# Kernel tuning notes

Hardware: AMD Instinct MI355X
Metric: run time of the kernel (lower is better)

Reference implementation:

```python
import jax, jax.numpy as jnp
import numpy as np

B, T, C, HS = 8, 4096, 128, 64
NEG_INF = -1e30  # stand-in for float('-inf') that is fp16/bf16-safe


def _rope(x, cos, sin):
    # x: [B, T, HS]; cos/sin: [T, HS//2]
    xr = x.reshape(*x.shape[:-1], HS // 2, 2)
    x0, x1 = xr[..., 0], xr[..., 1]
    # complex multiply (x0 + i x1) * (cos + i sin)
    o0 = x0 * cos - x1 * sin
    o1 = x0 * sin + x1 * cos
    return jnp.stack([o0, o1], axis=-1).reshape(x.shape)


def setup_inputs() -> dict:
    key = jax.random.key(0)
    k0, k1, k2, k3, k4 = jax.random.split(key, 5)
    x_text_emb = jax.random.normal(k0, (B, T, C), dtype=jnp.float32)
    Wq = jax.random.normal(k1, (C, HS), dtype=jnp.float32) * 0.02
    Wk = jax.random.normal(k2, (C, HS), dtype=jnp.float32) * 0.02
    Wv = jax.random.normal(k3, (C, HS), dtype=jnp.float32) * 0.02
    # RoPE frequencies: theta_i = 10000^{-2i/HS}, angles = pos * theta
    theta = 10000.0 ** (-jnp.arange(0, HS, 2, dtype=jnp.float32) / HS)  # [HS//2]
    angles = jnp.arange(T, dtype=jnp.float32)[:, None] * theta[None, :]  # [T, HS//2]
    freqs_cos = jnp.cos(angles)
    freqs_sin = jnp.sin(angles)
    # padding mask: ones for a valid prefix (length >= T//2 so no row is fully masked)
    lengths = jax.random.randint(k4, (B,), T // 2, T + 1)
    x_latex_mask = (jnp.arange(T)[None, :] < lengths[:, None]).astype(jnp.int32)
    return {"x_text_emb": x_text_emb, "Wq": Wq, "Wk": Wk, "Wv": Wv,
            "freqs_cos": freqs_cos, "freqs_sin": freqs_sin,
            "x_latex_mask": x_latex_mask}


def reference(x_text_emb, Wq, Wk, Wv, freqs_cos, freqs_sin, x_latex_mask):
    q = _rope(x_text_emb @ Wq, freqs_cos, freqs_sin)           # [B,T,HS]
    k = _rope(x_text_emb @ Wk, freqs_cos, freqs_sin)           # [B,T,HS]
    v = x_text_emb @ Wv                                        # [B,T,HS]
    # NOTE: source divides by sqrt(C) (embedding dim), not sqrt(head_size)
    wei = jnp.einsum('bqd,bkd->bqk', q, k) / jnp.sqrt(jnp.float32(C))  # [B,T,T]
    causal = jnp.tril(jnp.ones((T, T), dtype=bool))
    wei = jnp.where(causal[None, :, :], wei, NEG_INF)
    wei = jnp.where(x_latex_mask[:, None, :] != 0, wei, NEG_INF)
    softwei = jax.nn.softmax(wei, axis=-1)
    return jnp.einsum('bqk,bkd->bqd', softwei, v)              # [B,T,HS]
```

## Files before the change

kernel.cpp:

```cpp
#include <hip/hip_runtime.h>

#define B_ 8
#define T_ 4096
#define C_ 128
#define HS_ 64
#define NT16 (T_ / 16)

typedef _Float16 f16;
typedef _Float16 f16x8 __attribute__((ext_vector_type(8)));
typedef _Float16 f16x4 __attribute__((ext_vector_type(4)));
typedef float f32x4 __attribute__((ext_vector_type(4)));

#define MFMA32(a, b, c) __builtin_amdgcn_mfma_f32_16x16x32_f16(a, b, c, 0, 0, 0)
#define MFMA16(a, b, c) __builtin_amdgcn_mfma_f32_16x16x16f16(a, b, c, 0, 0, 0)


__global__ void k_prep(const float* __restrict__ Wq, const float* __restrict__ Wk,
                       const float* __restrict__ Wv, const int* __restrict__ msk,
                       f16* __restrict__ WT, f16* __restrict__ bias) {
    int idx = blockIdx.x * 256 + threadIdx.x;
    if (idx < 192 * C_) {
        int j = idx >> 7, c = idx & 127;
        const float* W = (j < 64) ? Wq : (j < 128 ? Wk : Wv);
        float v = W[c * HS_ + (j & 63)];
        if (j < 64) v *= 0.08838834764831845f;
        WT[idx] = (f16)v;
    } else {
        int e = idx - 192 * C_;
        if (e < B_ * T_) bias[e] = msk[e] ? (f16)0.0f : (f16)(-30000.0f);
    }
}

__global__ __launch_bounds__(256, 2) void k_qkv(const float* __restrict__ x,
        const f16* __restrict__ WT, const float* __restrict__ fcos,
        const float* __restrict__ fsin, f16* __restrict__ Qf,
        f16* __restrict__ Kf, f16* __restrict__ Vf) {
    const int b = blockIdx.y;
    const int tile64 = blockIdx.x >> 1, jh = blockIdx.x & 1;
    const int w = threadIdx.x >> 6, lane = threadIdx.x & 63;
    const int col = lane & 15, g = lane >> 4;
    const int t = tile64 * 64 + w * 16 + col;
    const int t16 = tile64 * 4 + w;
    const size_t fbase = ((size_t)(b * NT16) + t16) * 1024;

    f16x8 bx[4];
    const float* xrow = x + ((size_t)(b * T_ + t)) * C_;
#pragma unroll
    for (int cc = 0; cc < 4; ++cc) {
        float4 x0 = *(const float4*)(xrow + cc * 32 + g * 8);
        float4 x1 = *(const float4*)(xrow + cc * 32 + g * 8 + 4);
        f16x8 v;
        v[0] = (f16)x0.x; v[1] = (f16)x0.y; v[2] = (f16)x0.z; v[3] = (f16)x0.w;
        v[4] = (f16)x1.x; v[5] = (f16)x1.y; v[6] = (f16)x1.z; v[7] = (f16)x1.w;
        bx[cc] = v;
    }

#pragma unroll
    for (int jj = 0; jj < 6; ++jj) {
        const int jt = jh * 6 + jj;
        f32x4 acc = {0.f, 0.f, 0.f, 0.f};
#pragma unroll
        for (int cc = 0; cc < 4; ++cc) {
            f16x8 aw = *(const f16x8*)(WT + (size_t)(jt * 16 + col) * C_ + cc * 32 + g * 8);
            acc = MFMA32(aw, bx[cc], acc);
        }
        if (jt < 8) {
            const int j3 = jt & 3;
            const int hbase = j3 * 16 + g * 4;
            const int i0 = hbase >> 1;
            float2 c2 = *(const float2*)(fcos + t * 32 + i0);
            float2 s2 = *(const float2*)(fsin + t * 32 + i0);
            float o0 = acc[0] * c2.x - acc[1] * s2.x;
            float o1 = acc[0] * s2.x + acc[1] * c2.x;
            float o2 = acc[2] * c2.y - acc[3] * s2.y;
            float o3 = acc[2] * s2.y + acc[3] * c2.y;
            f16x4 st; st[0] = (f16)o0; st[1] = (f16)o1; st[2] = (f16)o2; st[3] = (f16)o3;
            const int h  = j3 >> 1;
            const int ga = ((j3 & 1) << 1) + (g >> 1);
            f16* dst = (jt < 4 ? Qf : Kf) + fbase + h * 512 + (ga * 16 + col) * 8 + (g & 1) * 4;
            *(f16x4*)dst = st;
        } else {
            const int mt = jt - 8;
            f16* vdst = Vf + fbase + mt * 256 + ((col >> 2) * 16 + g * 4) * 4 + (col & 3);
#pragma unroll
            for (int r = 0; r < 4; ++r) vdst[r * 4] = (f16)acc[r];
        }
    }
}

struct Tile32 {
    f16x8 k0[2], k1[2];
    f16x4 v[2][4];
    f16x4 bi[2];
};

__device__ __forceinline__ void load32(Tile32& t_, int it, const f16* __restrict__ kfb,
        const f16* __restrict__ vfb, const f16* __restrict__ brow, int lid, int g) {
#pragma unroll
    for (int s = 0; s < 2; ++s) {
        const f16* kt = kfb + (size_t)(it * 2 + s) * 1024;
        t_.k0[s] = *(const f16x8*)(kt + lid * 8);
        t_.k1[s] = *(const f16x8*)(kt + 512 + lid * 8);
        const f16* vt = vfb + (size_t)(it * 2 + s) * 1024;
#pragma unroll
        for (int mt = 0; mt < 4; ++mt)
            t_.v[s][mt] = *(const f16x4*)(vt + mt * 256 + lid * 4);
        t_.bi[s] = *(const f16x4*)(brow + it * 32 + s * 16 + g * 4);
    }
}

__device__ __forceinline__ void computeG(const Tile32& t_, int it, int qc, int g,
        f16x8 q0, f16x8 q1, float& m, float& lsum,
        f32x4& o0, f32x4& o1, f32x4& o2, f32x4& o3) {
    float sv[8];
#pragma unroll
    for (int s = 0; s < 2; ++s) {
        f32x4 sa = {0.f, 0.f, 0.f, 0.f};
        sa = MFMA32(t_.k0[s], q0, sa);
        sa = MFMA32(t_.k1[s], q1, sa);
        const int kbase = it * 32 + s * 16 + g * 4;
#pragma unroll
        for (int r = 0; r < 4; ++r) {
            float bb = (kbase + r <= qc) ? (float)t_.bi[s][r] : -1e30f;
            sv[s * 4 + r] = sa[r] + bb;
        }
    }
    float t0 = fmaxf(fmaxf(sv[0], sv[1]), fmaxf(sv[2], sv[3]));
    float t1 = fmaxf(fmaxf(sv[4], sv[5]), fmaxf(sv[6], sv[7]));
    float tm = fmaxf(t0, t1);
    tm = fmaxf(tm, __shfl_xor(tm, 16));
    tm = fmaxf(tm, __shfl_xor(tm, 32));
    const float mn = fmaxf(m, tm);
    const float sc = __expf(m - mn);
#pragma unroll
    for (int i = 0; i < 8; ++i) sv[i] = __expf(sv[i] - mn);
    float ts = ((sv[0] + sv[1]) + (sv[2] + sv[3])) + ((sv[4] + sv[5]) + (sv[6] + sv[7]));
    ts += __shfl_xor(ts, 16);
    ts += __shfl_xor(ts, 32);
    lsum = lsum * sc + ts;
    m = mn;
    o0 *= sc; o1 *= sc; o2 *= sc; o3 *= sc;
#pragma unroll
    for (int s = 0; s < 2; ++s) {
        f16x4 pf;
        pf[0] = (f16)sv[s * 4 + 0]; pf[1] = (f16)sv[s * 4 + 1];
        pf[2] = (f16)sv[s * 4 + 2]; pf[3] = (f16)sv[s * 4 + 3];
        o0 = MFMA16(t_.v[s][0], pf, o0);
        o1 = MFMA16(t_.v[s][1], pf, o1);
        o2 = MFMA16(t_.v[s][2], pf, o2);
        o3 = MFMA16(t_.v[s][3], pf, o3);
    }
}

__device__ __forceinline__ void writeG(float* __restrict__ out, int b, int qc, int g,
        float lsum, const f32x4& o0, const f32x4& o1, const f32x4& o2, const f32x4& o3) {
    const float inv = 1.0f / lsum;
    float* orow = out + ((size_t)(b * T_ + qc)) * HS_;
    float4 u;
    u.x = o0.x * inv; u.y = o0.y * inv; u.z = o0.z * inv; u.w = o0.w * inv;
    *(float4*)(orow + 0  + g * 4) = u;
    u.x = o1.x * inv; u.y = o1.y * inv; u.z = o1.z * inv; u.w = o1.w * inv;
    *(float4*)(orow + 16 + g * 4) = u;
    u.x = o2.x * inv; u.y = o2.y * inv; u.z = o2.z * inv; u.w = o2.w * inv;
    *(float4*)(orow + 32 + g * 4) = u;
    u.x = o3.x * inv; u.y = o3.y * inv; u.z = o3.z * inv; u.w = o3.w * inv;
    *(float4*)(orow + 48 + g * 4) = u;
}

__global__ __launch_bounds__(256, 1) void k_attn(const f16* __restrict__ Qf,
        const f16* __restrict__ Kf, const f16* __restrict__ Vf,
        const f16* __restrict__ bias, float* __restrict__ out) {
    const int b = blockIdx.y;
    const int xx = blockIdx.x;
    const int w = threadIdx.x >> 6, lane = threadIdx.x & 63;
    const int col = lane & 15, g = lane >> 4;
    const int lid = g * 16 + col;
    const int tqA = xx, tqB = 63 - xx;
    const int qcA = tqA * 64 + w * 16 + col;
    const int qcB = tqB * 64 + w * 16 + col;
    const int itA = (tqA * 64 + w * 16 + 15) >> 5;
    const int itB = (tqB * 64 + w * 16 + 15) >> 5;

    const f16* qfb = Qf + (size_t)(b * NT16) * 1024;
    const f16* kfb = Kf + (size_t)(b * NT16) * 1024;
    const f16* vfb = Vf + (size_t)(b * NT16) * 1024;
    const f16* brow = bias + (size_t)b * T_;

    const f16* qA = qfb + (size_t)(tqA * 4 + w) * 1024;
    f16x8 qA0 = *(const f16x8*)(qA + lid * 8);
    f16x8 qA1 = *(const f16x8*)(qA + 512 + lid * 8);
    const f16* qB = qfb + (size_t)(tqB * 4 + w) * 1024;
    f16x8 qB0 = *(const f16x8*)(qB + lid * 8);
    f16x8 qB1 = *(const f16x8*)(qB + 512 + lid * 8);

    float mA = -3.0e38f, lA = 0.f, mB = -3.0e38f, lB = 0.f;
    f32x4 oA0 = {0,0,0,0}, oA1 = {0,0,0,0}, oA2 = {0,0,0,0}, oA3 = {0,0,0,0};
    f32x4 oB0 = {0,0,0,0}, oB1 = {0,0,0,0}, oB2 = {0,0,0,0}, oB3 = {0,0,0,0};

    Tile32 A, Bt;
    load32(A, 0, kfb, vfb, brow, lid, g);
    int it = 0;
    for (; it + 2 <= itB; it += 2) {
        load32(Bt, it + 1, kfb, vfb, brow, lid, g);
        if (it <= itA) computeG(A, it, qcA, g, qA0, qA1, mA, lA, oA0, oA1, oA2, oA3);
        computeG(A, it, qcB, g, qB0, qB1, mB, lB, oB0, oB1, oB2, oB3);
        load32(A, it + 2, kfb, vfb, brow, lid, g);
        if (it + 1 <= itA) computeG(Bt, it + 1, qcA, g, qA0, qA1, mA, lA, oA0, oA1, oA2, oA3);
        computeG(Bt, it + 1, qcB, g, qB0, qB1, mB, lB, oB0, oB1, oB2, oB3);
    }
    if (it < itB) {
        load32(Bt, it + 1, kfb, vfb, brow, lid, g);
        if (it <= itA) computeG(A, it, qcA, g, qA0, qA1, mA, lA, oA0, oA1, oA2, oA3);
        computeG(A, it, qcB, g, qB0, qB1, mB, lB, oB0, oB1, oB2, oB3);
        if (it + 1 <= itA) computeG(Bt, it + 1, qcA, g, qA0, qA1, mA, lA, oA0, oA1, oA2, oA3);
        computeG(Bt, it + 1, qcB, g, qB0, qB1, mB, lB, oB0, oB1, oB2, oB3);
    } else {
        if (it <= itA) computeG(A, it, qcA, g, qA0, qA1, mA, lA, oA0, oA1, oA2, oA3);
        computeG(A, it, qcB, g, qB0, qB1, mB, lB, oB0, oB1, oB2, oB3);
    }

    writeG(out, b, qcA, g, lA, oA0, oA1, oA2, oA3);
    writeG(out, b, qcB, g, lB, oB0, oB1, oB2, oB3);
}

extern "C" void kernel_launch(void* const* d_in, const int* in_sizes, int n_in,
                              void* d_out, int out_size, void* d_ws, size_t ws_size,
                              hipStream_t stream) {
    const float* x    = (const float*)d_in[0];
    const float* Wq   = (const float*)d_in[1];
    const float* Wk   = (const float*)d_in[2];
    const float* Wv   = (const float*)d_in[3];
    const float* fcos = (const float*)d_in[4];
    const float* fsin = (const float*)d_in[5];
    const int*   msk  = (const int*)d_in[6];

    char* ws = (char*)d_ws;
    const size_t frag_bytes = (size_t)B_ * NT16 * 2048;
    f16* WT   = (f16*)ws;
    f16* bias = (f16*)(ws + (48 << 10));
    f16* Qf   = (f16*)(ws + (1 << 17));
    f16* Kf   = (f16*)(ws + (1 << 17) + frag_bytes);
    f16* Vf   = (f16*)(ws + (1 << 17) + 2 * frag_bytes);

    k_prep<<<224, 256, 0, stream>>>(Wq, Wk, Wv, msk, WT, bias);
    dim3 g1(T_ / 32, B_);
    k_qkv<<<g1, 256, 0, stream>>>(x, WT, fcos, fsin, Qf, Kf, Vf);
    dim3 g2(32, B_);
    k_attn<<<g2, 256, 0, stream>>>(Qf, Kf, Vf, bias, (float*)d_out);
}
```

Measured before the change: 171.7 us.

## Split KV range across waves in attention, stage QKV inputs in LDS

The attention kernel now launches 1024-thread blocks where each wave handles one query tile and half of its key range, merging the two partial softmax states through shared memory. This raises wave count and parallelism compared with two query tiles per wave processed serially. Along with this, the causal mask is applied only on the last key tile, and output rescaling is skipped when the running max does not change. The QKV projection now stages x and the weights in swizzled LDS, computes all 12 output tiles per block, and writes V through an LDS transpose for coalesced stores. The price is extra LDS use and a block-wide sync, and the attention loop no longer double-buffers its loads.

```diff
diff --git a/kernel.cpp b/kernel.cpp
--- a/kernel.cpp
+++ b/kernel.cpp
@@ -35,33 +35,57 @@
         const f16* __restrict__ WT, const float* __restrict__ fcos,
         const float* __restrict__ fsin, f16* __restrict__ Qf,
         f16* __restrict__ Kf, f16* __restrict__ Vf) {
+    __shared__ f16 xs[64 * 128];
+    __shared__ f16 wts[192 * 128];
+    __shared__ f16 vst[4][4][256];
+
     const int b = blockIdx.y;
-    const int tile64 = blockIdx.x >> 1, jh = blockIdx.x & 1;
-    const int w = threadIdx.x >> 6, lane = threadIdx.x & 63;
+    const int tid = threadIdx.x;
+    const int w = tid >> 6, lane = tid & 63;
     const int col = lane & 15, g = lane >> 4;
-    const int t = tile64 * 64 + w * 16 + col;
-    const int t16 = tile64 * 4 + w;
+
+    const float* xb = x + ((size_t)b * T_ + (size_t)blockIdx.x * 64) * C_;
+#pragma unroll
+    for (int k = 0; k < 8; ++k) {
+        int flat = tid * 4 + k * 1024;
+        float4 v4 = *(const float4*)(xb + flat);
+        f16x4 hv; hv[0] = (f16)v4.x; hv[1] = (f16)v4.y; hv[2] = (f16)v4.z; hv[3] = (f16)v4.w;
+        int row = flat >> 7, chB = (flat & 127) * 2;
+        int off = (row * 256 + chB) ^ ((row & 7) << 4);
+        *(f16x4*)((char*)xs + off) = hv;
+    }
+#pragma unroll
+    for (int k = 0; k < 12; ++k) {
+        int flat = tid * 8 + k * 2048;
+        f16x8 wv = *(const f16x8*)(WT + flat);
+        int row = flat >> 7, chB = (flat & 127) * 2;
+        int off = (row * 256 + chB) ^ ((row & 7) << 4);
+        *(f16x8*)((char*)wts + off) = wv;
+    }
+    __syncthreads();
+
+    const int t = blockIdx.x * 64 + w * 16 + col;
+    const int t16 = blockIdx.x * 4 + w;
     const size_t fbase = ((size_t)(b * NT16) + t16) * 1024;
 
     f16x8 bx[4];
-    const float* xrow = x + ((size_t)(b * T_ + t)) * C_;
-#pragma unroll
-    for (int cc = 0; cc < 4; ++cc) {
-        float4 x0 = *(const float4*)(xrow + cc * 32 + g * 8);
-        float4 x1 = *(const float4*)(xrow + cc * 32 + g * 8 + 4);
-        f16x8 v;
-        v[0] = (f16)x0.x; v[1] = (f16)x0.y; v[2] = (f16)x0.z; v[3] = (f16)x0.w;
-        v[4] = (f16)x1.x; v[5] = (f16)x1.y; v[6] = (f16)x1.z; v[7] = (f16)x1.w;
-        bx[cc] = v;
-    }
-
-#pragma unroll
-    for (int jj = 0; jj < 6; ++jj) {
-        const int jt = jh * 6 + jj;
+    {
+        const int row = w * 16 + col;
+#pragma unroll
+        for (int cc = 0; cc < 4; ++cc) {
+            int off = (row * 256 + cc * 64 + g * 16) ^ ((row & 7) << 4);
+            bx[cc] = *(const f16x8*)((const char*)xs + off);
+        }
+    }
+
+#pragma unroll
+    for (int jt = 0; jt < 12; ++jt) {
         f32x4 acc = {0.f, 0.f, 0.f, 0.f};
+        const int wrow = jt * 16 + col;
 #pragma unroll
         for (int cc = 0; cc < 4; ++cc) {
-            f16x8 aw = *(const f16x8*)(WT + (size_t)(jt * 16 + col) * C_ + cc * 32 + g * 8);
+            int off = (wrow * 256 + cc * 64 + g * 16) ^ ((wrow & 7) << 4);
+            f16x8 aw = *(const f16x8*)((const char*)wts + off);
             acc = MFMA32(aw, bx[cc], acc);
         }
         if (jt < 8) {
@@ -75,16 +99,27 @@
             float o2 = acc[2] * c2.y - acc[3] * s2.y;
             float o3 = acc[2] * s2.y + acc[3] * c2.y;
             f16x4 st; st[0] = (f16)o0; st[1] = (f16)o1; st[2] = (f16)o2; st[3] = (f16)o3;
-            const int h  = j3 >> 1;
+            const int hh = j3 >> 1;
             const int ga = ((j3 & 1) << 1) + (g >> 1);
-            f16* dst = (jt < 4 ? Qf : Kf) + fbase + h * 512 + (ga * 16 + col) * 8 + (g & 1) * 4;
+            f16* dst = (jt < 4 ? Qf : Kf) + fbase + hh * 512 + (ga * 16 + col) * 8 + (g & 1) * 4;
             *(f16x4*)dst = st;
         } else {
             const int mt = jt - 8;
-            f16* vdst = Vf + fbase + mt * 256 + ((col >> 2) * 16 + g * 4) * 4 + (col & 3);
-#pragma unroll
-            for (int r = 0; r < 4; ++r) vdst[r * 4] = (f16)acc[r];
-        }
+#pragma unroll
+            for (int r = 0; r < 4; ++r) {
+                int F = (col >> 2) * 64 + (g * 4 + r) * 4 + (col & 3);
+                int Bl = F * 2;
+                Bl ^= ((Bl >> 7) & 3) << 4;
+                *(f16*)((char*)&vst[w][mt][0] + Bl) = (f16)acc[r];
+            }
+        }
+    }
+#pragma unroll
+    for (int mt = 0; mt < 4; ++mt) {
+        int Bl = lane * 8;
+        Bl ^= ((Bl >> 7) & 3) << 4;
+        f16x4 vv = *(const f16x4*)((const char*)&vst[w][mt][0] + Bl);
+        *(f16x4*)(Vf + fbase + mt * 256 + lane * 4) = vv;
     }
 }
 
@@ -95,22 +130,22 @@
 };
 
 __device__ __forceinline__ void load32(Tile32& t_, int it, const f16* __restrict__ kfb,
-        const f16* __restrict__ vfb, const f16* __restrict__ brow, int lid, int g) {
+        const f16* __restrict__ vfb, const f16* __restrict__ brow, int lane, int g) {
 #pragma unroll
     for (int s = 0; s < 2; ++s) {
         const f16* kt = kfb + (size_t)(it * 2 + s) * 1024;
-        t_.k0[s] = *(const f16x8*)(kt + lid * 8);
-        t_.k1[s] = *(const f16x8*)(kt + 512 + lid * 8);
+        t_.k0[s] = *(const f16x8*)(kt + lane * 8);
+        t_.k1[s] = *(const f16x8*)(kt + 512 + lane * 8);
         const f16* vt = vfb + (size_t)(it * 2 + s) * 1024;
 #pragma unroll
         for (int mt = 0; mt < 4; ++mt)
-            t_.v[s][mt] = *(const f16x4*)(vt + mt * 256 + lid * 4);
+            t_.v[s][mt] = *(const f16x4*)(vt + mt * 256 + lane * 4);
         t_.bi[s] = *(const f16x4*)(brow + it * 32 + s * 16 + g * 4);
     }
 }
 
-__device__ __forceinline__ void computeG(const Tile32& t_, int it, int qc, int g,
-        f16x8 q0, f16x8 q1, float& m, float& lsum,
+__device__ __forceinline__ void computeG(const Tile32& t_, int it, bool last,
+        int qc, int g, f16x8 q0, f16x8 q1, float& m, float& lsum,
         f32x4& o0, f32x4& o1, f32x4& o2, f32x4& o3) {
     float sv[8];
 #pragma unroll
@@ -121,7 +156,8 @@
         const int kbase = it * 32 + s * 16 + g * 4;
 #pragma unroll
         for (int r = 0; r < 4; ++r) {
-            float bb = (kbase + r <= qc) ? (float)t_.bi[s][r] : -1e30f;
+            float bb = (float)t_.bi[s][r];
+            if (last) bb = (kbase + r <= qc) ? bb : -1e30f;
             sv[s * 4 + r] = sa[r] + bb;
         }
     }
@@ -130,16 +166,21 @@
     float tm = fmaxf(t0, t1);
     tm = fmaxf(tm, __shfl_xor(tm, 16));
     tm = fmaxf(tm, __shfl_xor(tm, 32));
-    const float mn = fmaxf(m, tm);
-    const float sc = __expf(m - mn);
+    const bool skip = __all(tm <= m);
+    const float mn = skip ? m : fmaxf(m, tm);
 #pragma unroll
     for (int i = 0; i < 8; ++i) sv[i] = __expf(sv[i] - mn);
     float ts = ((sv[0] + sv[1]) + (sv[2] + sv[3])) + ((sv[4] + sv[5]) + (sv[6] + sv[7]));
     ts += __shfl_xor(ts, 16);
     ts += __shfl_xor(ts, 32);
-    lsum = lsum * sc + ts;
-    m = mn;
-    o0 *= sc; o1 *= sc; o2 *= sc; o3 *= sc;
+    if (skip) {
+        lsum += ts;
+    } else {
+        const float sc = __expf(m - mn);
+        lsum = lsum * sc + ts;
+        m = mn;
+        o0 *= sc; o1 *= sc; o2 *= sc; o3 *= sc;
+    }
 #pragma unroll
     for (int s = 0; s < 2; ++s) {
         f16x4 pf;
@@ -152,75 +193,75 @@
     }
 }
 
-__device__ __forceinline__ void writeG(float* __restrict__ out, int b, int qc, int g,
-        float lsum, const f32x4& o0, const f32x4& o1, const f32x4& o2, const f32x4& o3) {
-    const float inv = 1.0f / lsum;
-    float* orow = out + ((size_t)(b * T_ + qc)) * HS_;
-    float4 u;
-    u.x = o0.x * inv; u.y = o0.y * inv; u.z = o0.z * inv; u.w = o0.w * inv;
-    *(float4*)(orow + 0  + g * 4) = u;
-    u.x = o1.x * inv; u.y = o1.y * inv; u.z = o1.z * inv; u.w = o1.w * inv;
-    *(float4*)(orow + 16 + g * 4) = u;
-    u.x = o2.x * inv; u.y = o2.y * inv; u.z = o2.z * inv; u.w = o2.w * inv;
-    *(float4*)(orow + 32 + g * 4) = u;
-    u.x = o3.x * inv; u.y = o3.y * inv; u.z = o3.z * inv; u.w = o3.w * inv;
-    *(float4*)(orow + 48 + g * 4) = u;
-}
-
-__global__ __launch_bounds__(256, 1) void k_attn(const f16* __restrict__ Qf,
+__global__ __launch_bounds__(1024, 4) void k_attn(const f16* __restrict__ Qf,
         const f16* __restrict__ Kf, const f16* __restrict__ Vf,
         const f16* __restrict__ bias, float* __restrict__ out) {
+    __shared__ float lds_o[8][64][17];
+    __shared__ float lds_m[8][64];
+    __shared__ float lds_l[8][64];
+
     const int b = blockIdx.y;
     const int xx = blockIdx.x;
     const int w = threadIdx.x >> 6, lane = threadIdx.x & 63;
     const int col = lane & 15, g = lane >> 4;
-    const int lid = g * 16 + col;
-    const int tqA = xx, tqB = 63 - xx;
-    const int qcA = tqA * 64 + w * 16 + col;
-    const int qcB = tqB * 64 + w * 16 + col;
-    const int itA = (tqA * 64 + w * 16 + 15) >> 5;
-    const int itB = (tqB * 64 + w * 16 + 15) >> 5;
+    const int h = w & 1, r = (w >> 1) & 3, side = w >> 3;
+    const int tq = side ? (63 - xx) : xx;
+    const int qc = tq * 64 + r * 16 + col;
+    const int itLast = (tq * 64 + r * 16 + 15) >> 5;
+    const int LA = itLast + 1, mid = LA >> 1;
+    const int start = h ? mid : 0, endEx = h ? LA : mid;
+    const int slot = side * 4 + r;
 
     const f16* qfb = Qf + (size_t)(b * NT16) * 1024;
     const f16* kfb = Kf + (size_t)(b * NT16) * 1024;
     const f16* vfb = Vf + (size_t)(b * NT16) * 1024;
     const f16* brow = bias + (size_t)b * T_;
 
-    const f16* qA = qfb + (size_t)(tqA * 4 + w) * 1024;
-    f16x8 qA0 = *(const f16x8*)(qA + lid * 8);
-    f16x8 qA1 = *(const f16x8*)(qA + 512 + lid * 8);
-    const f16* qB = qfb + (size_t)(tqB * 4 + w) * 1024;
-    f16x8 qB0 = *(const f16x8*)(qB + lid * 8);
-    f16x8 qB1 = *(const f16x8*)(qB + 512 + lid * 8);
-
-    float mA = -3.0e38f, lA = 0.f, mB = -3.0e38f, lB = 0.f;
-    f32x4 oA0 = {0,0,0,0}, oA1 = {0,0,0,0}, oA2 = {0,0,0,0}, oA3 = {0,0,0,0};
-    f32x4 oB0 = {0,0,0,0}, oB1 = {0,0,0,0}, oB2 = {0,0,0,0}, oB3 = {0,0,0,0};
-
-    Tile32 A, Bt;
-    load32(A, 0, kfb, vfb, brow, lid, g);
-    int it = 0;
-    for (; it + 2 <= itB; it += 2) {
-        load32(Bt, it + 1, kfb, vfb, brow, lid, g);
-        if (it <= itA) computeG(A, it, qcA, g, qA0, qA1, mA, lA, oA0, oA1, oA2, oA3);
-        computeG(A, it, qcB, g, qB0, qB1, mB, lB, oB0, oB1, oB2, oB3);
-        load32(A, it + 2, kfb, vfb, brow, lid, g);
-        if (it + 1 <= itA) computeG(Bt, it + 1, qcA, g, qA0, qA1, mA, lA, oA0, oA1, oA2, oA3);
-        computeG(Bt, it + 1, qcB, g, qB0, qB1, mB, lB, oB0, oB1, oB2, oB3);
-    }
-    if (it < itB) {
-        load32(Bt, it + 1, kfb, vfb, brow, lid, g);
-        if (it <= itA) computeG(A, it, qcA, g, qA0, qA1, mA, lA, oA0, oA1, oA2, oA3);
-        computeG(A, it, qcB, g, qB0, qB1, mB, lB, oB0, oB1, oB2, oB3);
-        if (it + 1 <= itA) computeG(Bt, it + 1, qcA, g, qA0, qA1, mA, lA, oA0, oA1, oA2, oA3);
-        computeG(Bt, it + 1, qcB, g, qB0, qB1, mB, lB, oB0, oB1, oB2, oB3);
-    } else {
-        if (it <= itA) computeG(A, it, qcA, g, qA0, qA1, mA, lA, oA0, oA1, oA2, oA3);
-        computeG(A, it, qcB, g, qB0, qB1, mB, lB, oB0, oB1, oB2, oB3);
-    }
-
-    writeG(out, b, qcA, g, lA, oA0, oA1, oA2, oA3);
-    writeG(out, b, qcB, g, lB, oB0, oB1, oB2, oB3);
+    const f16* qp = qfb + (size_t)(tq * 4 + r) * 1024;
+    f16x8 q0 = *(const f16x8*)(qp + lane * 8);
+    f16x8 q1 = *(const f16x8*)(qp + 512 + lane * 8);
+
+    float m = -3.0e38f, lsum = 0.f;
+    f32x4 o0 = {0,0,0,0}, o1 = {0,0,0,0}, o2 = {0,0,0,0}, o3 = {0,0,0,0};
+
+    for (int it = start; it < endEx; ++it) {
+        Tile32 tl;
+        load32(tl, it, kfb, vfb, brow, lane, g);
+        computeG(tl, it, it == itLast, qc, g, q0, q1, m, lsum, o0, o1, o2, o3);
+    }
+
+    if (h) {
+        lds_m[slot][lane] = m;
+        lds_l[slot][lane] = lsum;
+        float* p = lds_o[slot][lane];
+        p[0] = o0.x;  p[1] = o0.y;  p[2] = o0.z;  p[3] = o0.w;
+        p[4] = o1.x;  p[5] = o1.y;  p[6] = o1.z;  p[7] = o1.w;
+        p[8] = o2.x;  p[9] = o2.y;  p[10] = o2.z; p[11] = o2.w;
+        p[12] = o3.x; p[13] = o3.y; p[14] = o3.z; p[15] = o3.w;
+    }
+    __syncthreads();
+    if (!h) {
+        const float mB = lds_m[slot][lane];
+        const float lB = lds_l[slot][lane];
+        const float mn = fmaxf(m, mB);
+        const float sA = __expf(m - mn), sB = __expf(mB - mn);
+        const float inv = 1.0f / (lsum * sA + lB * sB);
+        const float* p = lds_o[slot][lane];
+        float* orow = out + ((size_t)(b * T_ + qc)) * HS_;
+        float4 u;
+        u.x = (o0.x * sA + p[0] * sB) * inv;  u.y = (o0.y * sA + p[1] * sB) * inv;
+        u.z = (o0.z * sA + p[2] * sB) * inv;  u.w = (o0.w * sA + p[3] * sB) * inv;
+        *(float4*)(orow + 0  + g * 4) = u;
+        u.x = (o1.x * sA + p[4] * sB) * inv;  u.y = (o1.y * sA + p[5] * sB) * inv;
+        u.z = (o1.z * sA + p[6] * sB) * inv;  u.w = (o1.w * sA + p[7] * sB) * inv;
+        *(float4*)(orow + 16 + g * 4) = u;
+        u.x = (o2.x * sA + p[8] * sB) * inv;  u.y = (o2.y * sA + p[9] * sB) * inv;
+        u.z = (o2.z * sA + p[10] * sB) * inv; u.w = (o2.w * sA + p[11] * sB) * inv;
+        *(float4*)(orow + 32 + g * 4) = u;
+        u.x = (o3.x * sA + p[12] * sB) * inv; u.y = (o3.y * sA + p[13] * sB) * inv;
+        u.z = (o3.z * sA + p[14] * sB) * inv; u.w = (o3.w * sA + p[15] * sB) * inv;
+        *(float4*)(orow + 48 + g * 4) = u;
+    }
 }
 
 extern "C" void kernel_launch(void* const* d_in, const int* in_sizes, int n_in,
@@ -243,8 +284,8 @@
     f16* Vf   = (f16*)(ws + (1 << 17) + 2 * frag_bytes);
 
     k_prep<<<224, 256, 0, stream>>>(Wq, Wk, Wv, msk, WT, bias);
-    dim3 g1(T_ / 32, B_);
+    dim3 g1(T_ / 64, B_);
     k_qkv<<<g1, 256, 0, stream>>>(x, WT, fcos, fsin, Qf, Kf, Vf);
     dim3 g2(32, B_);
-    k_attn<<<g2, 256, 0, stream>>>(Qf, Kf, Vf, bias, (float*)d_out);
-}
+    k_attn<<<g2, 1024, 0, stream>>>(Qf, Kf, Vf, bias, (float*)d_out);
+}
```

Measured after the change: 144.6 us. -15.8%, faster.
